# Optimization experiments

Hardware: AMD Instinct MI355X
Metric: run time of the kernel (lower is better)

The kernel has to match this reference:

```python
import jax, jax.numpy as jnp
import numpy as np
import math

INPUT_DIM = 256
HIDDEN_DIM = 128
N = 8192
GATE_TEMPERATURE = 1.0
LN_EPS = 1e-5


def setup_inputs() -> dict:
    key = jax.random.key(0)
    ks = jax.random.split(key, 10)
    s_in = 1.0 / math.sqrt(INPUT_DIM)
    s_h = 1.0 / math.sqrt(HIDDEN_DIM)
    s_cat = 1.0 / math.sqrt(INPUT_DIM + HIDDEN_DIM)
    return {
        "node_features": jax.random.normal(ks[0], (N, INPUT_DIM), jnp.float32),
        "adj_matrix": jax.random.uniform(ks[1], (N, N), jnp.float32),
        "msg_w": jax.random.uniform(ks[2], (INPUT_DIM, HIDDEN_DIM), jnp.float32, -s_in, s_in),
        "msg_b": jax.random.uniform(ks[3], (HIDDEN_DIM,), jnp.float32, -s_in, s_in),
        "upd_w": jax.random.uniform(ks[4], (INPUT_DIM + HIDDEN_DIM, HIDDEN_DIM), jnp.float32, -s_cat, s_cat),
        "upd_b": jax.random.uniform(ks[5], (HIDDEN_DIM,), jnp.float32, -s_cat, s_cat),
        "gate_q_w": jax.random.uniform(ks[6], (HIDDEN_DIM, HIDDEN_DIM), jnp.float32, -s_h, s_h),
        "gate_k_w": jax.random.uniform(ks[7], (HIDDEN_DIM, HIDDEN_DIM), jnp.float32, -s_h, s_h),
        "gate_bias": jnp.float32(-1.0),
        "ln_gamma": jnp.ones((HIDDEN_DIM,), jnp.float32),
        "ln_beta": jnp.zeros((HIDDEN_DIM,), jnp.float32),
    }


def reference(node_features, adj_matrix, msg_w, msg_b, upd_w, upd_b,
              gate_q_w, gate_k_w, gate_bias, ln_gamma, ln_beta):
    # messages: [N, hidden]
    messages = node_features @ msg_w + msg_b
    # edge gates: sigmoid(QK^T / (sqrt(d)*tau) + b), masked by adjacency
    q = messages @ gate_q_w  # [N, hidden]
    k = messages @ gate_k_w  # [N, hidden]
    scale = 1.0 / (math.sqrt(HIDDEN_DIM) * max(GATE_TEMPERATURE, 1e-6))
    scores = (q @ k.T) * scale  # [N, N]
    gates_masked = jax.nn.sigmoid(scores + gate_bias) * adj_matrix
    aggregated = gates_masked @ messages  # [N, hidden]
    combined = jnp.concatenate([node_features, aggregated], axis=1)
    updated = jax.nn.relu(combined @ upd_w + upd_b)
    # LayerNorm over last dim
    mu = jnp.mean(updated, axis=-1, keepdims=True)
    var = jnp.var(updated, axis=-1, keepdims=True)
    normed = (updated - mu) * jax.lax.rsqrt(var + LN_EPS)
    return normed * ln_gamma + ln_beta
```

## Files before the change

### kernel.cpp

```cpp
#include <hip/hip_runtime.h>
#include <hip/hip_bf16.h>
#include <stdint.h>

#define NN 8192
#define DIN 256
#define HID 128
#define SCALE 0.08838834764831845f

typedef __attribute__((ext_vector_type(8))) short short8;
typedef __attribute__((ext_vector_type(4))) float f32x4;
typedef __attribute__((ext_vector_type(8))) unsigned short u16x8;
typedef __attribute__((ext_vector_type(4))) unsigned short u16x4;

__device__ __forceinline__ unsigned short f2bf(float f) {
  unsigned int u = __builtin_bit_cast(unsigned int, f);
  u += 0x7FFFu + ((u >> 16) & 1u);
  return (unsigned short)(u >> 16);
}

__device__ __forceinline__ void async16(const void* g, void* l) {
  __builtin_amdgcn_global_load_lds(
      (const __attribute__((address_space(1))) unsigned int*)g,
      (__attribute__((address_space(3))) unsigned int*)l, 16, 0, 0);
}

__global__ __launch_bounds__(256) void kw0(
    const float* __restrict__ msg_w, const float* __restrict__ qw,
    const float* __restrict__ kw, const float* __restrict__ upd_w,
    unsigned short* __restrict__ mwT, unsigned short* __restrict__ qwT,
    unsigned short* __restrict__ kwT, unsigned short* __restrict__ w_t) {
  int idx0 = blockIdx.x * 1792 + threadIdx.x;
#pragma unroll
  for (int it = 0; it < 7; ++it) {
    int idx = idx0 + it * 256;
    if (idx < 32768) {
      int h = idx >> 8, j = idx & 255;
      mwT[idx] = f2bf(msg_w[j * HID + h]);
    } else if (idx < 49152) {
      int r = idx - 32768, h = r >> 7, j = r & 127;
      qwT[r] = f2bf(qw[j * HID + h]);
    } else if (idx < 65536) {
      int r = idx - 49152, h = r >> 7, j = r & 127;
      kwT[r] = f2bf(kw[j * HID + h]);
    } else {
      int r = idx - 65536, h = r / 384, j = r % 384;
      w_t[r] = f2bf(upd_w[j * HID + h]);
    }
  }
}

__global__ __launch_bounds__(256) void ka(
    const float* __restrict__ nf, const unsigned short* __restrict__ mwT,
    const float* __restrict__ msg_b, const unsigned short* __restrict__ qwT,
    const unsigned short* __restrict__ kwT, unsigned short* __restrict__ q_bf,
    unsigned short* __restrict__ k_bf, unsigned short* __restrict__ m_t,
    unsigned short* __restrict__ nf_bf) {
  __shared__ __align__(16) unsigned short nfl[32][264];
  __shared__ __align__(16) unsigned short ml[32][136];
  int t = threadIdx.x, l = t & 63, w = t >> 6;
  int lr = l & 15, lg = l >> 4;
  int i0 = blockIdx.x * 32;
  {
    int row = t >> 3, c0 = (t & 7) * 32;
    const float* src = nf + (size_t)(i0 + row) * DIN + c0;
    unsigned short* gdst = nf_bf + (size_t)(i0 + row) * DIN + c0;
#pragma unroll
    for (int v = 0; v < 4; ++v) {
      f32x4 a = *(const f32x4*)(src + v * 8);
      f32x4 b = *(const f32x4*)(src + v * 8 + 4);
      u16x8 o;
#pragma unroll
      for (int e = 0; e < 4; ++e) { o[e] = f2bf(a[e]); o[4 + e] = f2bf(b[e]); }
      *(u16x8*)&nfl[row][c0 + v * 8] = o;
      *(u16x8*)(gdst + v * 8) = o;
    }
  }
  __syncthreads();
  int rl = (w >> 1) * 16;
  int nb = (w & 1) * 4;
  f32x4 macc[4];
#pragma unroll
  for (int nt = 0; nt < 4; ++nt) macc[nt] = (f32x4){0.f, 0.f, 0.f, 0.f};
#pragma unroll
  for (int kk = 0; kk < 8; ++kk) {
    short8 af = *(const short8*)&nfl[rl + lr][kk * 32 + lg * 8];
#pragma unroll
    for (int nt = 0; nt < 4; ++nt) {
      short8 bf = *(const short8*)(mwT + (size_t)((nb + nt) * 16 + lr) * DIN + kk * 32 + lg * 8);
      macc[nt] = __builtin_amdgcn_mfma_f32_16x16x32_bf16(af, bf, macc[nt], 0, 0, 0);
    }
  }
#pragma unroll
  for (int nt = 0; nt < 4; ++nt) {
    int col = (nb + nt) * 16 + lr;
    float bias = msg_b[col];
#pragma unroll
    for (int reg = 0; reg < 4; ++reg)
      ml[rl + lg * 4 + reg][col] = f2bf(macc[nt][reg] + bias);
  }
  __syncthreads();
  {
    int hh = t >> 1, i8 = (t & 1) * 16;
    u16x8 o0, o1;
#pragma unroll
    for (int v = 0; v < 8; ++v) { o0[v] = ml[i8 + v][hh]; o1[v] = ml[i8 + 8 + v][hh]; }
    *(u16x8*)(m_t + (size_t)hh * NN + i0 + i8) = o0;
    *(u16x8*)(m_t + (size_t)hh * NN + i0 + i8 + 8) = o1;
  }
  f32x4 qacc[4], kacc[4];
#pragma unroll
  for (int nt = 0; nt < 4; ++nt) {
    qacc[nt] = (f32x4){0.f, 0.f, 0.f, 0.f};
    kacc[nt] = (f32x4){0.f, 0.f, 0.f, 0.f};
  }
#pragma unroll
  for (int kk = 0; kk < 4; ++kk) {
    short8 af = *(const short8*)&ml[rl + lr][kk * 32 + lg * 8];
#pragma unroll
    for (int nt = 0; nt < 4; ++nt) {
      short8 bq = *(const short8*)(qwT + (size_t)((nb + nt) * 16 + lr) * HID + kk * 32 + lg * 8);
      short8 bk = *(const short8*)(kwT + (size_t)((nb + nt) * 16 + lr) * HID + kk * 32 + lg * 8);
      qacc[nt] = __builtin_amdgcn_mfma_f32_16x16x32_bf16(af, bq, qacc[nt], 0, 0, 0);
      kacc[nt] = __builtin_amdgcn_mfma_f32_16x16x32_bf16(af, bk, kacc[nt], 0, 0, 0);
    }
  }
#pragma unroll
  for (int nt = 0; nt < 4; ++nt) {
    int col = (nb + nt) * 16 + lr;
#pragma unroll
    for (int reg = 0; reg < 4; ++reg) {
      int row = i0 + rl + lg * 4 + reg;
      q_bf[(size_t)row * HID + col] = f2bf(qacc[nt][reg]);
      k_bf[(size_t)row * HID + col] = f2bf(kacc[nt][reg]);
    }
  }
}

__global__ __launch_bounds__(256, 4) void kb(
    const unsigned short* __restrict__ q_bf, const unsigned short* __restrict__ k_bf,
    const unsigned short* __restrict__ m_t, const float* __restrict__ adj,
    const float* __restrict__ gate_bias, float* __restrict__ agg_parts) {
  __shared__ __align__(16) char klds[16384];
  __shared__ __align__(16) char mlds[16384];
  __shared__ __align__(16) char glds[8192];
  int t = threadIdx.x, l = t & 63, w = t >> 6;
  int lr = l & 15, lg = l >> 4;
  int lin = blockIdx.x + blockIdx.y * 128;
  int nlin = (lin & 7) * 128 + (lin >> 3);
  int bx = nlin & 127, by = nlin >> 7;
  int i0 = bx * 64;
  int jbase = by * 1024;
  float gb = gate_bias[0];

  int qrow = i0 + w * 16 + lr;
  short8 qf[4];
#pragma unroll
  for (int kk = 0; kk < 4; ++kk)
    qf[kk] = *(const short8*)(q_bf + (size_t)qrow * HID + kk * 32 + lg * 8);

  int krow = t >> 4;
  int klb = (t & 15) ^ (krow & 7);
  int mrow_s = t >> 3;
  int mlb = (t & 7) ^ (mrow_s & 7);

  const float* arow[4];
#pragma unroll
  for (int reg = 0; reg < 4; ++reg)
    arow[reg] = adj + (size_t)(i0 + w * 16 + lg * 4 + reg) * NN + lr;

  f32x4 acc[8];
#pragma unroll
  for (int nt = 0; nt < 8; ++nt) acc[nt] = (f32x4){0.f, 0.f, 0.f, 0.f};

  float adjv[2][4][4];
#pragma unroll
  for (int jt16 = 0; jt16 < 4; ++jt16)
#pragma unroll
    for (int reg = 0; reg < 4; ++reg)
      adjv[0][jt16][reg] = arow[reg][jbase + jt16 * 16];

#pragma unroll 2
  for (int jt = 0; jt < 16; ++jt) {
    const int cur = jt & 1;
    int j0 = jbase + jt * 64;
#pragma unroll
    for (int p = 0; p < 4; ++p)
      async16(k_bf + (size_t)(j0 + p * 16 + krow) * HID + klb * 8,
              klds + p * 4096 + w * 1024);
#pragma unroll
    for (int p = 0; p < 4; ++p)
      async16(m_t + (size_t)(p * 32 + mrow_s) * NN + j0 + mlb * 8,
              mlds + p * 4096 + w * 1024);
    asm volatile("" ::: "memory");
    {
      int jn0 = jbase + (jt < 15 ? jt + 1 : jt) * 64;
#pragma unroll
      for (int jt16 = 0; jt16 < 4; ++jt16)
#pragma unroll
        for (int reg = 0; reg < 4; ++reg)
          adjv[cur ^ 1][jt16][reg] = arow[reg][jn0 + jt16 * 16];
    }
    asm volatile("s_waitcnt vmcnt(16)" ::: "memory");
    __builtin_amdgcn_s_barrier();

#pragma unroll
    for (int jt16 = 0; jt16 < 4; ++jt16) {
      f32x4 s_acc = (f32x4){0.f, 0.f, 0.f, 0.f};
#pragma unroll
      for (int kk = 0; kk < 4; ++kk) {
        int row = jt16 * 16 + lr;
        int blk = kk * 4 + lg;
        const short8 bf = *(const short8*)(klds + row * 256 + ((blk ^ (row & 7)) * 16));
        s_acc = __builtin_amdgcn_mfma_f32_16x16x32_bf16(qf[kk], bf, s_acc, 0, 0, 0);
      }
#pragma unroll
      for (int reg = 0; reg < 4; ++reg) {
        float x = s_acc[reg] * SCALE + gb;
        float e = __expf(-x);
        float g = adjv[cur][jt16][reg] * __builtin_amdgcn_rcpf(1.0f + e);
        int row = lg * 4 + reg;
        int colb = (jt16 * 16 + lr) * 2;
        *(unsigned short*)(glds + w * 2048 + row * 128 + (colb ^ ((row & 7) << 4))) =
            f2bf(g);
      }
    }
#pragma unroll
    for (int kk2 = 0; kk2 < 2; ++kk2) {
      short8 af = *(const short8*)(glds + w * 2048 + lr * 128 +
                                   ((kk2 * 64 + lg * 16) ^ ((lr & 7) << 4)));
#pragma unroll
      for (int nt = 0; nt < 8; ++nt) {
        int mrow = nt * 16 + lr;
        int blk = kk2 * 4 + lg;
        const short8 bf =
            *(const short8*)(mlds + mrow * 128 + ((blk ^ (mrow & 7)) * 16));
        acc[nt] = __builtin_amdgcn_mfma_f32_16x16x32_bf16(af, bf, acc[nt], 0, 0, 0);
      }
    }
    __builtin_amdgcn_s_barrier();
  }
  float* part = agg_parts + (size_t)by * NN * HID;
#pragma unroll
  for (int nt = 0; nt < 8; ++nt)
#pragma unroll
    for (int reg = 0; reg < 4; ++reg)
      part[(size_t)(i0 + w * 16 + lg * 4 + reg) * HID + nt * 16 + lr] = acc[nt][reg];
}

__global__ __launch_bounds__(256) void kc(
    const unsigned short* __restrict__ nf_bf, const float* __restrict__ agg_parts,
    const unsigned short* __restrict__ w_t, const float* __restrict__ upd_b,
    const float* __restrict__ gamma, const float* __restrict__ beta,
    float* __restrict__ out) {
  __shared__ __align__(16) unsigned short aggl[64][136];
  int t = threadIdx.x, l = t & 63, w = t >> 6;
  int i0 = blockIdx.x * 64;
  {
    const f32x4* p0 = (const f32x4*)(agg_parts + (size_t)i0 * HID);
    const size_t ps = (size_t)NN * HID / 4;
    for (int e = t; e < 64 * HID / 4; e += 256) {
      f32x4 s = p0[e];
#pragma unroll
      for (int c = 1; c < 8; ++c) s += p0[e + c * ps];
      int row = (e * 4) / HID, col = (e * 4) % HID;
      u16x4 o;
#pragma unroll
      for (int v = 0; v < 4; ++v) o[v] = f2bf(s[v]);
      *(u16x4*)&aggl[row][col] = o;
    }
  }
  __syncthreads();
  int lr = l & 15, lg = l >> 4;
  int arow = i0 + w * 16 + lr;
  short8 af[12];
#pragma unroll
  for (int kk = 0; kk < 8; ++kk)
    af[kk] = *(const short8*)(nf_bf + (size_t)arow * DIN + kk * 32 + lg * 8);
#pragma unroll
  for (int kk = 8; kk < 12; ++kk)
    af[kk] = *(const short8*)(&aggl[w * 16 + lr][(kk - 8) * 32 + lg * 8]);
  f32x4 acc[8];
#pragma unroll
  for (int nt = 0; nt < 8; ++nt) acc[nt] = (f32x4){0.f, 0.f, 0.f, 0.f};
#pragma unroll
  for (int kk = 0; kk < 12; ++kk)
#pragma unroll
    for (int nt = 0; nt < 8; ++nt) {
      const short8 bf =
          *(const short8*)(w_t + (size_t)(nt * 16 + lr) * 384 + kk * 32 + lg * 8);
      acc[nt] = __builtin_amdgcn_mfma_f32_16x16x32_bf16(af[kk], bf, acc[nt], 0, 0, 0);
    }
  float ub[8], ga[8], be[8];
#pragma unroll
  for (int nt = 0; nt < 8; ++nt) {
    ub[nt] = upd_b[nt * 16 + lr];
    ga[nt] = gamma[nt * 16 + lr];
    be[nt] = beta[nt * 16 + lr];
  }
  float v[8][4], sum[4], sq[4];
#pragma unroll
  for (int reg = 0; reg < 4; ++reg) { sum[reg] = 0.f; sq[reg] = 0.f; }
#pragma unroll
  for (int nt = 0; nt < 8; ++nt)
#pragma unroll
    for (int reg = 0; reg < 4; ++reg) {
      float x = acc[nt][reg] + ub[nt];
      x = fmaxf(x, 0.f);
      v[nt][reg] = x;
      sum[reg] += x;
      sq[reg] = fmaf(x, x, sq[reg]);
    }
#pragma unroll
  for (int reg = 0; reg < 4; ++reg) {
#pragma unroll
    for (int m = 1; m < 16; m <<= 1) {
      sum[reg] += __shfl_xor(sum[reg], m, 16);
      sq[reg] += __shfl_xor(sq[reg], m, 16);
    }
  }
#pragma unroll
  for (int reg = 0; reg < 4; ++reg) {
    float mu = sum[reg] * (1.0f / 128.0f);
    float var = sq[reg] * (1.0f / 128.0f) - mu * mu;
    float rstd = rsqrtf(var + 1e-5f);
    int orow = i0 + w * 16 + lg * 4 + reg;
#pragma unroll
    for (int nt = 0; nt < 8; ++nt) {
      float y = (v[nt][reg] - mu) * rstd * ga[nt] + be[nt];
      out[(size_t)orow * HID + nt * 16 + lr] = y;
    }
  }
}

extern "C" void kernel_launch(void* const* d_in, const int* in_sizes, int n_in,
                              void* d_out, int out_size, void* d_ws, size_t ws_size,
                              hipStream_t stream) {
  const float* nf    = (const float*)d_in[0];
  const float* adj   = (const float*)d_in[1];
  const float* msg_w = (const float*)d_in[2];
  const float* msg_b = (const float*)d_in[3];
  const float* upd_w = (const float*)d_in[4];
  const float* upd_b = (const float*)d_in[5];
  const float* qw    = (const float*)d_in[6];
  const float* kw    = (const float*)d_in[7];
  const float* gbias = (const float*)d_in[8];
  const float* gamma = (const float*)d_in[9];
  const float* beta  = (const float*)d_in[10];
  char* ws = (char*)d_ws;
  unsigned short* q_bf  = (unsigned short*)(ws);
  unsigned short* k_bf  = (unsigned short*)(ws + 0x200000);
  unsigned short* m_t   = (unsigned short*)(ws + 0x400000);
  unsigned short* nf_bf = (unsigned short*)(ws + 0x600000);
  unsigned short* w_t   = (unsigned short*)(ws + 0xA00000);
  unsigned short* mwT   = (unsigned short*)(ws + 0xA20000);
  unsigned short* qwT   = (unsigned short*)(ws + 0xA30000);
  unsigned short* kwT   = (unsigned short*)(ws + 0xA38000);
  float* agg            = (float*)(ws + 0xA40000);

  kw0<<<64, 256, 0, stream>>>(msg_w, qw, kw, upd_w, mwT, qwT, kwT, w_t);
  ka<<<256, 256, 0, stream>>>(nf, mwT, msg_b, qwT, kwT, q_bf, k_bf, m_t, nf_bf);
  kb<<<dim3(128, 8), 256, 0, stream>>>(q_bf, k_bf, m_t, adj, gbias, agg);
  kc<<<128, 256, 0, stream>>>(nf_bf, agg, w_t, upd_b, gamma, beta, (float*)d_out);
}
```

Before: 146.9 us.

## Double-buffer K and message LDS tiles with next-tile async prefetch

Result: faster. 142.0 us (-3.3%).

```diff
diff --git a/kernel.cpp b/kernel.cpp
--- a/kernel.cpp
+++ b/kernel.cpp
@@ -136,12 +136,12 @@
   }
 }
 
-__global__ __launch_bounds__(256, 4) void kb(
+__global__ __launch_bounds__(256, 2) void kb(
     const unsigned short* __restrict__ q_bf, const unsigned short* __restrict__ k_bf,
     const unsigned short* __restrict__ m_t, const float* __restrict__ adj,
     const float* __restrict__ gate_bias, float* __restrict__ agg_parts) {
-  __shared__ __align__(16) char klds[16384];
-  __shared__ __align__(16) char mlds[16384];
+  __shared__ __align__(16) char klds[2][16384];
+  __shared__ __align__(16) char mlds[2][16384];
   __shared__ __align__(16) char glds[8192];
   int t = threadIdx.x, l = t & 63, w = t >> 6;
   int lr = l & 15, lg = l >> 4;
@@ -172,36 +172,46 @@
 #pragma unroll
   for (int nt = 0; nt < 8; ++nt) acc[nt] = (f32x4){0.f, 0.f, 0.f, 0.f};
 
-  float adjv[2][4][4];
-#pragma unroll
-  for (int jt16 = 0; jt16 < 4; ++jt16)
-#pragma unroll
-    for (int reg = 0; reg < 4; ++reg)
-      adjv[0][jt16][reg] = arow[reg][jbase + jt16 * 16];
-
-#pragma unroll 2
-  for (int jt = 0; jt < 16; ++jt) {
-    const int cur = jt & 1;
-    int j0 = jbase + jt * 64;
+  {
+    int j0 = jbase;
 #pragma unroll
     for (int p = 0; p < 4; ++p)
       async16(k_bf + (size_t)(j0 + p * 16 + krow) * HID + klb * 8,
-              klds + p * 4096 + w * 1024);
+              &klds[0][p * 4096 + w * 1024]);
 #pragma unroll
     for (int p = 0; p < 4; ++p)
       async16(m_t + (size_t)(p * 32 + mrow_s) * NN + j0 + mlb * 8,
-              mlds + p * 4096 + w * 1024);
+              &mlds[0][p * 4096 + w * 1024]);
+  }
+
+  for (int jt = 0; jt < 16; ++jt) {
+    int j0 = jbase + jt * 64;
+    const char* kcur = &klds[jt & 1][0];
+    const char* mcur = &mlds[jt & 1][0];
+    float adjv[4][4];
+#pragma unroll
+    for (int jt16 = 0; jt16 < 4; ++jt16)
+#pragma unroll
+      for (int reg = 0; reg < 4; ++reg)
+        adjv[jt16][reg] = arow[reg][j0 + jt16 * 16];
     asm volatile("" ::: "memory");
     {
-      int jn0 = jbase + (jt < 15 ? jt + 1 : jt) * 64;
-#pragma unroll
-      for (int jt16 = 0; jt16 < 4; ++jt16)
-#pragma unroll
-        for (int reg = 0; reg < 4; ++reg)
-          adjv[cur ^ 1][jt16][reg] = arow[reg][jn0 + jt16 * 16];
-    }
-    asm volatile("s_waitcnt vmcnt(16)" ::: "memory");
+      int jn = (jt + 1) & 15;
+      int j0n = jbase + jn * 64;
+      char* knxt = &klds[(jt + 1) & 1][0];
+      char* mnxt = &mlds[(jt + 1) & 1][0];
+#pragma unroll
+      for (int p = 0; p < 4; ++p)
+        async16(k_bf + (size_t)(j0n + p * 16 + krow) * HID + klb * 8,
+                knxt + p * 4096 + w * 1024);
+#pragma unroll
+      for (int p = 0; p < 4; ++p)
+        async16(m_t + (size_t)(p * 32 + mrow_s) * NN + j0n + mlb * 8,
+                mnxt + p * 4096 + w * 1024);
+    }
+    asm volatile("s_waitcnt vmcnt(24)" ::: "memory");
     __builtin_amdgcn_s_barrier();
+    __builtin_amdgcn_sched_barrier(0);
 
 #pragma unroll
     for (int jt16 = 0; jt16 < 4; ++jt16) {
@@ -210,14 +220,14 @@
       for (int kk = 0; kk < 4; ++kk) {
         int row = jt16 * 16 + lr;
         int blk = kk * 4 + lg;
-        const short8 bf = *(const short8*)(klds + row * 256 + ((blk ^ (row & 7)) * 16));
+        const short8 bf = *(const short8*)(kcur + row * 256 + ((blk ^ (row & 7)) * 16));
         s_acc = __builtin_amdgcn_mfma_f32_16x16x32_bf16(qf[kk], bf, s_acc, 0, 0, 0);
       }
 #pragma unroll
       for (int reg = 0; reg < 4; ++reg) {
         float x = s_acc[reg] * SCALE + gb;
         float e = __expf(-x);
-        float g = adjv[cur][jt16][reg] * __builtin_amdgcn_rcpf(1.0f + e);
+        float g = adjv[jt16][reg] * __builtin_amdgcn_rcpf(1.0f + e);
         int row = lg * 4 + reg;
         int colb = (jt16 * 16 + lr) * 2;
         *(unsigned short*)(glds + w * 2048 + row * 128 + (colb ^ ((row & 7) << 4))) =
@@ -233,10 +243,11 @@
         int mrow = nt * 16 + lr;
         int blk = kk2 * 4 + lg;
         const short8 bf =
-            *(const short8*)(mlds + mrow * 128 + ((blk ^ (mrow & 7)) * 16));
+            *(const short8*)(mcur + mrow * 128 + ((blk ^ (mrow & 7)) * 16));
         acc[nt] = __builtin_amdgcn_mfma_f32_16x16x32_bf16(af, bf, acc[nt], 0, 0, 0);
       }
     }
+    __builtin_amdgcn_sched_barrier(0);
     __builtin_amdgcn_s_barrier();
   }
   float* part = agg_parts + (size_t)by * NN * HID;
```
